# Kernel optimization log

Hardware: AMD Instinct MI355X
Metric: run time of the kernel (lower is better)

Reference implementation:

```python
import jax, jax.numpy as jnp
import numpy as np

DIM = 64
HID = 2 * DIM  # ffn_expansion_factor hard-coded to 2 in __init__


def _conv(x, w, b, pad, groups=1):
    # x: [N,C,H,W], w: [O, C//groups, kh, kw] (torch OIHW layout)
    y = jax.lax.conv_general_dilated(
        x, w, window_strides=(1, 1), padding=[(pad, pad), (pad, pad)],
        feature_group_count=groups,
        dimension_numbers=('NCHW', 'OIHW', 'NCHW'))
    return y + b[None, :, None, None]


def setup_inputs() -> dict:
    key = jax.random.key(0)
    ks = jax.random.split(key, 16)
    s = 0.05
    B, H, W = 4, 256, 256
    return {
        'x': jax.random.normal(ks[0], (B, DIM, H, W), jnp.float32),
        'pneffectiveness': jax.random.normal(ks[1], (B, 2, H, W), jnp.float32),
        # project_in: dim -> 2*hidden, 1x1
        'w_in': jax.random.normal(ks[2], (2 * HID, DIM, 1, 1), jnp.float32) * s,
        'b_in': jax.random.normal(ks[3], (2 * HID,), jnp.float32) * s,
        # project_in_pn: 2 -> hidden, 1x1
        'w_pn': jax.random.normal(ks[4], (HID, 2, 1, 1), jnp.float32) * s,
        'b_pn': jax.random.normal(ks[5], (HID,), jnp.float32) * s,
        # dwconvI: 3*hidden -> hidden, 3x3, groups=hidden (3 in-ch per group)
        'w_dw1': jax.random.normal(ks[6], (HID, 3, 3, 3), jnp.float32) * s,
        'b_dw1': jax.random.normal(ks[7], (HID,), jnp.float32) * s,
        # dwconvIII[0]: 3*hidden -> hidden, 3x3, groups=hidden
        'w_dw3a': jax.random.normal(ks[8], (HID, 3, 3, 3), jnp.float32) * s,
        'b_dw3a': jax.random.normal(ks[9], (HID,), jnp.float32) * s,
        # dwconvIII[1]: hidden -> hidden depthwise 3x3
        'w_dw3b': jax.random.normal(ks[10], (HID, 1, 3, 3), jnp.float32) * s,
        'b_dw3b': jax.random.normal(ks[11], (HID,), jnp.float32) * s,
        # project_out: hidden -> dim, 1x1, groups=2
        'w_out': jax.random.normal(ks[12], (DIM, HID // 2, 1, 1), jnp.float32) * s,
        'b_out': jax.random.normal(ks[13], (DIM,), jnp.float32) * s,
    }


def reference(x, pneffectiveness, w_in, b_in, w_pn, b_pn, w_dw1, b_dw1,
              w_dw3a, b_dw3a, w_dw3b, b_dw3b, w_out, b_out):
    xi = _conv(x, w_in, b_in, pad=0)                    # [B, 2*HID, H, W]
    pn = _conv(pneffectiveness, w_pn, b_pn, pad=0)      # [B, HID, H, W]
    xc = jnp.concatenate([pn, xi], axis=1)              # [B, 3*HID, H, W]
    d1 = _conv(xc, w_dw1, b_dw1, pad=1, groups=HID)     # [B, HID, H, W]
    d3 = _conv(xc, w_dw3a, b_dw3a, pad=1, groups=HID)
    d3 = _conv(d3, w_dw3b, b_dw3b, pad=1, groups=HID)   # [B, HID, H, W]
    x1_a, x1_b = jnp.split(d1, 2, axis=1)
    x2_a, x2_b = jnp.split(d3, 2, axis=1)
    x1 = jnp.concatenate([x1_a, x2_a], axis=1)          # [B, HID, H, W]
    x2 = jnp.concatenate([x1_b, x2_b], axis=1)
    g = jax.nn.gelu(x1, approximate=False) * x2         # exact GELU like F.gelu
    return _conv(g, w_out, b_out, pad=0, groups=2)      # [B, DIM, H, W]
```

## Files before the change

### kernel.cpp

```cpp
#include <hip/hip_runtime.h>
#include <hip/hip_bf16.h>


#define T 16
#define R20 20
#define R18 18
#define HW 65536
#define XC_BYTES ((size_t)4 * 16 * HW * 24 * 2)

typedef unsigned short u16;
typedef unsigned int u32;

typedef __attribute__((ext_vector_type(8))) short bf16x8;
typedef __attribute__((ext_vector_type(4))) float f32x4;

__device__ __forceinline__ float bflo(u32 w) {
    union { u32 i; float f; } v; v.i = w << 16; return v.f;
}
__device__ __forceinline__ float bfhi(u32 w) {
    union { u32 i; float f; } v; v.i = w & 0xffff0000u; return v.f;
}
__device__ __forceinline__ float bf2f(u16 u) {
    union { u32 i; float f; } v; v.i = ((u32)u) << 16; return v.f;
}
__device__ __forceinline__ u16 f2bf(float f) {
    union { float f; u32 i; } v; v.f = f;
    u32 x = v.i;
    u32 r = (x + 0x7fffu + ((x >> 16) & 1u)) >> 16;
    return (u16)r;
}
__device__ __forceinline__ float gelu_exact(float v) {
    return 0.5f * v * (1.0f + erff(v * 0.70710678118654752f));
}

__device__ __forceinline__ void pack_pair(float a, float b, u32& hi, u32& lo) {
    union { float f; u32 i; } ua, ub, ha, hb, la, lb;
    ua.f = a; ub.f = b;
    ha.i = ua.i & 0xffff0000u;
    hb.i = ub.i & 0xffff0000u;
    hi = (ha.i >> 16) | hb.i;
    la.f = a - ha.f;
    lb.f = b - hb.f;
    lo = (la.i >> 16) | (lb.i & 0xffff0000u);
}

__global__ __launch_bounds__(256, 2)
void k1_proj_mfma(const float* __restrict__ xin,
                  const float* __restrict__ pnin,
                  const float* __restrict__ w_in,
                  const float* __restrict__ b_in,
                  const float* __restrict__ w_pn,
                  const float* __restrict__ b_pn,
                  u16* __restrict__ xc)
{
    __shared__ float s_x[64][65];
    __shared__ __align__(16) u16 s_outT[64 * 388];
    __shared__ float s_bin[256];

    const int tid  = threadIdx.x;
    const int b    = blockIdx.y;
    const int px0  = blockIdx.x * 64;
    const int lane = tid & 63;
    const int wid  = tid >> 6;
    const int lr   = lane & 15;
    const int lh   = lane >> 4;
    const int CB   = wid * 64;

    s_bin[tid] = b_in[tid];

    {
        const float* xb = xin + (size_t)b * 64 * HW + px0;
#pragma unroll
        for (int i = 0; i < 4; ++i) {
            int idx = tid + 256 * i;
            int row = idx >> 4, seg = (idx & 15) * 4;
            float4 v = *(const float4*)(xb + (size_t)row * HW + seg);
            s_x[row][seg + 0] = v.x; s_x[row][seg + 1] = v.y;
            s_x[row][seg + 2] = v.z; s_x[row][seg + 3] = v.w;
        }
    }

    bf16x8 whi[4][2], wlo[4][2];
#pragma unroll
    for (int ci = 0; ci < 4; ++ci)
#pragma unroll
        for (int ks = 0; ks < 2; ++ks) {
            const float* wp = w_in + (size_t)(CB + 16 * ci + lr) * 64
                            + 32 * ks + 8 * lh;
            float4 A0 = *(const float4*)wp;
            float4 A1 = *(const float4*)(wp + 4);
            union { u32 u[4]; bf16x8 v; } H, L;
            pack_pair(A0.x, A0.y, H.u[0], L.u[0]);
            pack_pair(A0.z, A0.w, H.u[1], L.u[1]);
            pack_pair(A1.x, A1.y, H.u[2], L.u[2]);
            pack_pair(A1.z, A1.w, H.u[3], L.u[3]);
            whi[ci][ks] = H.v; wlo[ci][ks] = L.v;
        }

    {
        int px = tid & 63;
        float p0 = pnin[(size_t)b * 2 * HW + px0 + px];
        float p1 = pnin[(size_t)b * 2 * HW + HW + px0 + px];
        u16* orow = &s_outT[px * 388];
#pragma unroll
        for (int i = 0; i < 16; ++i) {
            int k = wid * 32 + 2 * i;
            float va = fmaf(w_pn[2 * k],     p0, fmaf(w_pn[2 * k + 1], p1, b_pn[k]));
            float vb = fmaf(w_pn[2 * k + 2], p0, fmaf(w_pn[2 * k + 3], p1, b_pn[k + 1]));
            *(u32*)&orow[k] = (u32)f2bf(va) | ((u32)f2bf(vb) << 16);
        }
    }
    __syncthreads();

    f32x4 acc[4][4];
#pragma unroll
    for (int ci = 0; ci < 4; ++ci)
#pragma unroll
        for (int pj = 0; pj < 4; ++pj)
            acc[ci][pj] = (f32x4){0.f, 0.f, 0.f, 0.f};

#pragma unroll
    for (int pj = 0; pj < 4; ++pj) {
        bf16x8 xh[2], xl[2];
#pragma unroll
        for (int ks = 0; ks < 2; ++ks) {
            const int rb = 32 * ks + 8 * lh;
            const int cb = 16 * pj + lr;
            float x0 = s_x[rb + 0][cb], x1 = s_x[rb + 1][cb];
            float x2 = s_x[rb + 2][cb], x3 = s_x[rb + 3][cb];
            float x4 = s_x[rb + 4][cb], x5 = s_x[rb + 5][cb];
            float x6 = s_x[rb + 6][cb], x7 = s_x[rb + 7][cb];
            union { u32 u[4]; bf16x8 v; } H, L;
            pack_pair(x0, x1, H.u[0], L.u[0]);
            pack_pair(x2, x3, H.u[1], L.u[1]);
            pack_pair(x4, x5, H.u[2], L.u[2]);
            pack_pair(x6, x7, H.u[3], L.u[3]);
            xh[ks] = H.v; xl[ks] = L.v;
        }
#pragma unroll
        for (int ci = 0; ci < 4; ++ci) {
#pragma unroll
            for (int ks = 0; ks < 2; ++ks) {
                acc[ci][pj] = __builtin_amdgcn_mfma_f32_16x16x32_bf16(
                    whi[ci][ks], xh[ks], acc[ci][pj], 0, 0, 0);
                acc[ci][pj] = __builtin_amdgcn_mfma_f32_16x16x32_bf16(
                    whi[ci][ks], xl[ks], acc[ci][pj], 0, 0, 0);
                acc[ci][pj] = __builtin_amdgcn_mfma_f32_16x16x32_bf16(
                    wlo[ci][ks], xh[ks], acc[ci][pj], 0, 0, 0);
            }
        }
    }

#pragma unroll
    for (int ci = 0; ci < 4; ++ci) {
        const int kk = CB + 16 * ci + 4 * lh;
        float b0 = s_bin[kk + 0], b1 = s_bin[kk + 1];
        float b2 = s_bin[kk + 2], b3 = s_bin[kk + 3];
#pragma unroll
        for (int pj = 0; pj < 4; ++pj) {
            f32x4 a = acc[ci][pj];
            int px = 16 * pj + lr;
            uint2 val;
            val.x = (u32)f2bf(a[0] + b0) | ((u32)f2bf(a[1] + b1) << 16);
            val.y = (u32)f2bf(a[2] + b2) | ((u32)f2bf(a[3] + b3) << 16);
            *(uint2*)&s_outT[px * 388 + 128 + kk] = val;
        }
    }
    __syncthreads();

    {
        const int c  = tid >> 4;
        const int pb = tid & 15;
#pragma unroll
        for (int rec = 0; rec < 4; ++rec) {
            int px = pb + 16 * rec;
            const u16* row = &s_outT[px * 388];
            const int k1o = 12 * c;
            const int k2o = 192 + 12 * c;
            uint2 a0 = *(const uint2*)&row[k1o];
            uint2 a1 = *(const uint2*)&row[k1o + 4];
            uint2 a2 = *(const uint2*)&row[k1o + 8];
            uint2 a3 = *(const uint2*)&row[k2o];
            uint2 a4 = *(const uint2*)&row[k2o + 4];
            uint2 a5 = *(const uint2*)&row[k2o + 8];
            uint4* dst = (uint4*)(xc + ((size_t)(b * 16 + c) * HW + px0 + px) * 24);
            dst[0] = make_uint4(a0.x, a0.y, a1.x, a1.y);
            dst[1] = make_uint4(a2.x, a2.y, a3.x, a3.y);
            dst[2] = make_uint4(a4.x, a4.y, a5.x, a5.y);
        }
    }
}

__global__ __launch_bounds__(512, 2)
void k2_spatial(const u16* __restrict__ xc,
                const float* __restrict__ w_dw1,  const float* __restrict__ b_dw1,
                const float* __restrict__ w_dw3a, const float* __restrict__ b_dw3a,
                const float* __restrict__ w_dw3b, const float* __restrict__ b_dw3b,
                const float* __restrict__ w_out,  const float* __restrict__ b_out,
                float* __restrict__ outp)
{
    __shared__ __align__(8) u16 s_xc[24][R20 * R20];
    __shared__ __align__(8) u16 s_d3a[8][R18 * R18];
    __shared__ __align__(8) u16 s_d1[8][T * T];
    __shared__ __align__(8) u16 s_d3[8][T * T];
    __shared__ float s_wout[64 * 64];
    __shared__ float s_wd1[8][27];
    __shared__ float s_wd3a[8][27];
    __shared__ float s_wd3b[8][9];
    __shared__ float s_b1[8], s_b3a[8], s_b3b[8];

    const int tid  = threadIdx.x;
    const int half = tid >> 8;
    const int pix  = tid & 255;
    const int ox0 = blockIdx.x * T;
    const int oy0 = blockIdx.y * T;
    const int b   = blockIdx.z;

    for (int i = tid; i < 4096; i += 512) s_wout[i] = w_out[i];

    float acc[32];
#pragma unroll
    for (int o = 0; o < 32; ++o) acc[o] = 0.f;

    for (int chunk = 0; chunk < 16; ++chunk) {
        const int c0 = chunk * 4;
        __syncthreads();

        {
            int t = tid;
            if (t < 216) {
                int gl = t / 27, idx = t - gl * 27;
                int g = (gl < 4) ? (c0 + gl) : (c0 + 60 + gl);
                s_wd1[gl][idx] = w_dw1[g * 27 + idx];
            } else if (t < 432) {
                int t2 = t - 216;
                int gl = t2 / 27, idx = t2 - gl * 27;
                int g = (gl < 4) ? (c0 + gl) : (c0 + 60 + gl);
                s_wd3a[gl][idx] = w_dw3a[g * 27 + idx];
            } else if (t < 504) {
                int t2 = t - 432;
                int gl = t2 / 9, idx = t2 - gl * 9;
                int g = (gl < 4) ? (c0 + gl) : (c0 + 60 + gl);
                s_wd3b[gl][idx] = w_dw3b[g * 9 + idx];
            } else if (t < 512) {
                int gl = t - 504;
                int g = (gl < 4) ? (c0 + gl) : (c0 + 60 + gl);
                s_b1[gl]  = b_dw1[g];
                s_b3a[gl] = b_dw3a[g];
                s_b3b[gl] = b_dw3b[g];
            }
        }

        if (tid < 400) {
            int py = tid / R20, px = tid - py * R20;
            int gy = oy0 - 2 + py, gx = ox0 - 2 + px;
            union { uint4 q[3]; u16 h[24]; } v;
            if ((unsigned)gy < 256u && (unsigned)gx < 256u) {
                const uint4* src = (const uint4*)(xc +
                    ((size_t)(b * 16 + chunk) * HW + gy * 256 + gx) * 24);
                v.q[0] = src[0]; v.q[1] = src[1]; v.q[2] = src[2];
            } else {
                v.q[0] = make_uint4(0, 0, 0, 0);
                v.q[1] = make_uint4(0, 0, 0, 0);
                v.q[2] = make_uint4(0, 0, 0, 0);
            }
#pragma unroll
            for (int l = 0; l < 24; ++l) s_xc[l][tid] = v.h[l];
        }
        __syncthreads();

        for (int task = tid; task < 8 * 81; task += 512) {
            int gl = task / 81, patch = task - gl * 81;
            int py = (patch / 9) * 2, px = (patch - (patch / 9) * 9) * 2;
            float bias = s_b3a[gl];
            float a00 = bias, a01 = bias, a10 = bias, a11 = bias;
#pragma unroll
            for (int j = 0; j < 3; ++j) {
                int lc = (gl < 4) ? (3 * gl + j) : (12 + 3 * (gl - 4) + j);
                const u32* base = (const u32*)&s_xc[lc][0];
                float win[4][4];
#pragma unroll
                for (int r = 0; r < 4; ++r) {
                    int e = (py + r) * R20 + px;
                    u32 u0 = base[e >> 1];
                    u32 u1 = base[(e >> 1) + 1];
                    win[r][0] = bflo(u0); win[r][1] = bfhi(u0);
                    win[r][2] = bflo(u1); win[r][3] = bfhi(u1);
                }
#pragma unroll
                for (int ky = 0; ky < 3; ++ky)
#pragma unroll
                    for (int kx = 0; kx < 3; ++kx) {
                        float wgt = s_wd3a[gl][j * 9 + ky * 3 + kx];
                        a00 = fmaf(wgt, win[ky][kx], a00);
                        a01 = fmaf(wgt, win[ky][kx + 1], a01);
                        a10 = fmaf(wgt, win[ky + 1][kx], a10);
                        a11 = fmaf(wgt, win[ky + 1][kx + 1], a11);
                    }
            }
            int gy0 = oy0 - 1 + py, gx0 = ox0 - 1 + px;
            bool vy0 = (unsigned)gy0 < 256u, vy1 = (unsigned)(gy0 + 1) < 256u;
            bool vx0 = (unsigned)gx0 < 256u, vx1 = (unsigned)(gx0 + 1) < 256u;
            u16* drow = &s_d3a[gl][py * R18 + px];
            drow[0]       = (vy0 && vx0) ? f2bf(a00) : (u16)0;
            drow[1]       = (vy0 && vx1) ? f2bf(a01) : (u16)0;
            drow[R18]     = (vy1 && vx0) ? f2bf(a10) : (u16)0;
            drow[R18 + 1] = (vy1 && vx1) ? f2bf(a11) : (u16)0;
        }

        {
            int gl = tid >> 6, patch = tid & 63;
            int py = (patch >> 3) * 2, px = (patch & 7) * 2;
            float bias = s_b1[gl];
            float a00 = bias, a01 = bias, a10 = bias, a11 = bias;
#pragma unroll
            for (int j = 0; j < 3; ++j) {
                int lc = (gl < 4) ? (3 * gl + j) : (12 + 3 * (gl - 4) + j);
                const u32* base = (const u32*)&s_xc[lc][0];
                float win[4][4];
#pragma unroll
                for (int r = 0; r < 4; ++r) {
                    int e = (py + 1 + r) * R20 + px;
                    u32 u0 = base[e >> 1];
                    u32 u1 = base[(e >> 1) + 1];
                    u32 u2 = base[(e >> 1) + 2];
                    win[r][0] = bfhi(u0); win[r][1] = bflo(u1);
                    win[r][2] = bfhi(u1); win[r][3] = bflo(u2);
                }
#pragma unroll
                for (int ky = 0; ky < 3; ++ky)
#pragma unroll
                    for (int kx = 0; kx < 3; ++kx) {
                        float wgt = s_wd1[gl][j * 9 + ky * 3 + kx];
                        a00 = fmaf(wgt, win[ky][kx], a00);
                        a01 = fmaf(wgt, win[ky][kx + 1], a01);
                        a10 = fmaf(wgt, win[ky + 1][kx], a10);
                        a11 = fmaf(wgt, win[ky + 1][kx + 1], a11);
                    }
            }
            u16* drow = &s_d1[gl][py * T + px];
            drow[0] = f2bf(a00); drow[1] = f2bf(a01);
            drow[T] = f2bf(a10); drow[T + 1] = f2bf(a11);
        }
        __syncthreads();

        {
            int gl = tid >> 6, patch = tid & 63;
            int py = (patch >> 3) * 2, px = (patch & 7) * 2;
            float bias = s_b3b[gl];
            float a00 = bias, a01 = bias, a10 = bias, a11 = bias;
            float win[4][4];
            const u32* base = (const u32*)&s_d3a[gl][0];
#pragma unroll
            for (int r = 0; r < 4; ++r) {
                int e = (py + r) * R18 + px;
                u32 u0 = base[e >> 1];
                u32 u1 = base[(e >> 1) + 1];
                win[r][0] = bflo(u0); win[r][1] = bfhi(u0);
                win[r][2] = bflo(u1); win[r][3] = bfhi(u1);
            }
#pragma unroll
            for (int ky = 0; ky < 3; ++ky)
#pragma unroll
                for (int kx = 0; kx < 3; ++kx) {
                    float wgt = s_wd3b[gl][ky * 3 + kx];
                    a00 = fmaf(wgt, win[ky][kx], a00);
                    a01 = fmaf(wgt, win[ky][kx + 1], a01);
                    a10 = fmaf(wgt, win[ky + 1][kx], a10);
                    a11 = fmaf(wgt, win[ky + 1][kx + 1], a11);
                }
            u16* drow = &s_d3[gl][py * T + px];
            drow[0] = f2bf(a00); drow[1] = f2bf(a01);
            drow[T] = f2bf(a10); drow[T + 1] = f2bf(a11);
        }
        __syncthreads();

        {
            const u16* sD = (half == 0) ? &s_d1[0][0] : &s_d3[0][0];
            const float* wrow = s_wout + half * 32 * 64;
#pragma unroll
            for (int jp = 0; jp < 2; ++jp) {
                int j0 = 2 * jp;
                float ga = gelu_exact(bf2f(sD[j0 * 256 + pix]))
                         * bf2f(sD[(j0 + 4) * 256 + pix]);
                float gb = gelu_exact(bf2f(sD[(j0 + 1) * 256 + pix]))
                         * bf2f(sD[(j0 + 5) * 256 + pix]);
                int c = c0 + j0;
#pragma unroll
                for (int o = 0; o < 32; ++o) {
                    float2 w2 = *(const float2*)(wrow + o * 64 + c);
                    acc[o] = fmaf(w2.x, ga, acc[o]);
                    acc[o] = fmaf(w2.y, gb, acc[o]);
                }
            }
        }
    }

    {
        int py = pix >> 4, pxx = pix & 15;
        size_t obase = (size_t)b * 64 * HW + (size_t)(half * 32) * HW
                     + (size_t)(oy0 + py) * 256 + (ox0 + pxx);
#pragma unroll
        for (int o = 0; o < 32; ++o)
            outp[obase + (size_t)o * HW] = acc[o] + b_out[half * 32 + o];
    }
}

__global__ __launch_bounds__(256, 2)
void ffd_fused(const float* __restrict__ xin, const float* __restrict__ pnin,
               const float* __restrict__ w_in, const float* __restrict__ b_in,
               const float* __restrict__ w_pn, const float* __restrict__ b_pn,
               const float* __restrict__ w_dw1, const float* __restrict__ b_dw1,
               const float* __restrict__ w_dw3a, const float* __restrict__ b_dw3a,
               const float* __restrict__ w_dw3b, const float* __restrict__ b_dw3b,
               const float* __restrict__ w_out, const float* __restrict__ b_out,
               float* __restrict__ outp)
{
    __shared__ __align__(8) u16 s_xc[24][R20 * R20];
    __shared__ __align__(8) float s_d3a[8][R18 * R18];
    __shared__ float s_d1[8][T * T];
    __shared__ float s_d3[8][T * T];
    __shared__ float s_wd1[8][27];
    __shared__ float s_wd3a[8][27];
    __shared__ float s_wd3b[8][9];
    __shared__ float s_b1[8], s_b3a[8], s_b3b[8];

    const int tid = threadIdx.x;
    const int ox0 = blockIdx.x * T;
    const int oy0 = blockIdx.y * T;
    const int b   = blockIdx.z;

    float accL[32], accH[32];
#pragma unroll
    for (int o = 0; o < 32; ++o) { accL[o] = 0.f; accH[o] = 0.f; }

    for (int chunk = 0; chunk < 16; ++chunk) {
        const int c0 = chunk * 4;
        __syncthreads();

        for (int t = tid; t < 512; t += 256) {
            if (t < 216) {
                int gl = t / 27, idx = t - gl * 27;
                int g = (gl < 4) ? (c0 + gl) : (c0 + 60 + gl);
                s_wd1[gl][idx] = w_dw1[g * 27 + idx];
            } else if (t < 432) {
                int t2 = t - 216;
                int gl = t2 / 27, idx = t2 - gl * 27;
                int g = (gl < 4) ? (c0 + gl) : (c0 + 60 + gl);
                s_wd3a[gl][idx] = w_dw3a[g * 27 + idx];
            } else if (t < 504) {
                int t2 = t - 432;
                int gl = t2 / 9, idx = t2 - gl * 9;
                int g = (gl < 4) ? (c0 + gl) : (c0 + 60 + gl);
                s_wd3b[gl][idx] = w_dw3b[g * 9 + idx];
            } else {
                int gl = t - 504;
                int g = (gl < 4) ? (c0 + gl) : (c0 + 60 + gl);
                s_b1[gl]  = b_dw1[g];
                s_b3a[gl] = b_dw3a[g];
                s_b3b[gl] = b_dw3b[g];
            }
        }

        for (int p = tid; p < R20 * R20; p += 256) {
            int py = p / R20, px = p - py * R20;
            int gy = oy0 - 2 + py, gx = ox0 - 2 + px;
            if ((unsigned)gy >= 256u || (unsigned)gx >= 256u) {
#pragma unroll 1
                for (int l = 0; l < 24; ++l) s_xc[l][p] = 0;
                continue;
            }
            const int off = gy * 256 + gx;
            float xr[64];
            const float* xp = xin + (size_t)b * 64 * HW + off;
#pragma unroll
            for (int c = 0; c < 64; ++c) xr[c] = xp[(size_t)c * HW];
            float p0 = 0.f, p1 = 0.f;
            if (3 * c0 < 128) {
                const float* pp = pnin + (size_t)b * 2 * HW + off;
                p0 = pp[0]; p1 = pp[HW];
            }
#pragma unroll 1
            for (int l = 0; l < 24; ++l) {
                int k = (l < 12) ? (3 * c0 + l) : (3 * c0 + 192 + (l - 12));
                float acc;
                if (k < 128) {
                    acc = b_pn[k] + w_pn[2 * k] * p0 + w_pn[2 * k + 1] * p1;
                } else {
                    int kk = k - 128;
                    acc = b_in[kk];
                    const float2* wr = (const float2*)(w_in + kk * 64);
#pragma unroll
                    for (int i = 0; i < 32; ++i) {
                        float2 w2 = wr[i];
                        acc = fmaf(w2.x, xr[2 * i], acc);
                        acc = fmaf(w2.y, xr[2 * i + 1], acc);
                    }
                }
                s_xc[l][p] = f2bf(acc);
            }
        }
        __syncthreads();

        for (int task = tid; task < 8 * 81; task += 256) {
            int gl = task / 81, patch = task - gl * 81;
            int py = (patch / 9) * 2, px = (patch - (patch / 9) * 9) * 2;
            float bias = s_b3a[gl];
            float a00 = bias, a01 = bias, a10 = bias, a11 = bias;
#pragma unroll
            for (int j = 0; j < 3; ++j) {
                int lc = (gl < 4) ? (3 * gl + j) : (12 + 3 * (gl - 4) + j);
                const u32* base = (const u32*)&s_xc[lc][0];
                float win[4][4];
#pragma unroll
                for (int r = 0; r < 4; ++r) {
                    int e = (py + r) * R20 + px;
                    u32 u0 = base[e >> 1];
                    u32 u1 = base[(e >> 1) + 1];
                    win[r][0] = bflo(u0); win[r][1] = bfhi(u0);
                    win[r][2] = bflo(u1); win[r][3] = bfhi(u1);
                }
#pragma unroll
                for (int ky = 0; ky < 3; ++ky)
#pragma unroll
                    for (int kx = 0; kx < 3; ++kx) {
                        float wgt = s_wd3a[gl][j * 9 + ky * 3 + kx];
                        a00 = fmaf(wgt, win[ky][kx], a00);
                        a01 = fmaf(wgt, win[ky][kx + 1], a01);
                        a10 = fmaf(wgt, win[ky + 1][kx], a10);
                        a11 = fmaf(wgt, win[ky + 1][kx + 1], a11);
                    }
            }
            int gy0 = oy0 - 1 + py, gx0 = ox0 - 1 + px;
            bool vy0 = (unsigned)gy0 < 256u, vy1 = (unsigned)(gy0 + 1) < 256u;
            bool vx0 = (unsigned)gx0 < 256u, vx1 = (unsigned)(gx0 + 1) < 256u;
            float* drow = &s_d3a[gl][py * R18 + px];
            drow[0]       = (vy0 && vx0) ? a00 : 0.f;
            drow[1]       = (vy0 && vx1) ? a01 : 0.f;
            drow[R18]     = (vy1 && vx0) ? a10 : 0.f;
            drow[R18 + 1] = (vy1 && vx1) ? a11 : 0.f;
        }

        for (int task = tid; task < 8 * 64; task += 256) {
            int gl = task >> 6, patch = task & 63;
            int py = (patch >> 3) * 2, px = (patch & 7) * 2;
            float bias = s_b1[gl];
            float a00 = bias, a01 = bias, a10 = bias, a11 = bias;
#pragma unroll
            for (int j = 0; j < 3; ++j) {
                int lc = (gl < 4) ? (3 * gl + j) : (12 + 3 * (gl - 4) + j);
                const u32* base = (const u32*)&s_xc[lc][0];
                float win[4][4];
#pragma unroll
                for (int r = 0; r < 4; ++r) {
                    int e = (py + 1 + r) * R20 + px;
                    u32 u0 = base[e >> 1];
                    u32 u1 = base[(e >> 1) + 1];
                    u32 u2 = base[(e >> 1) + 2];
                    win[r][0] = bfhi(u0); win[r][1] = bflo(u1);
                    win[r][2] = bfhi(u1); win[r][3] = bflo(u2);
                }
#pragma unroll
                for (int ky = 0; ky < 3; ++ky)
#pragma unroll
                    for (int kx = 0; kx < 3; ++kx) {
                        float wgt = s_wd1[gl][j * 9 + ky * 3 + kx];
                        a00 = fmaf(wgt, win[ky][kx], a00);
                        a01 = fmaf(wgt, win[ky][kx + 1], a01);
                        a10 = fmaf(wgt, win[ky + 1][kx], a10);
                        a11 = fmaf(wgt, win[ky + 1][kx + 1], a11);
                    }
            }
            float* drow = &s_d1[gl][py * T + px];
            drow[0] = a00; drow[1] = a01; drow[T] = a10; drow[T + 1] = a11;
        }
        __syncthreads();

        for (int task = tid; task < 8 * 64; task += 256) {
            int gl = task >> 6, patch = task & 63;
            int py = (patch >> 3) * 2, px = (patch & 7) * 2;
            float bias = s_b3b[gl];
            float a00 = bias, a01 = bias, a10 = bias, a11 = bias;
            float win[4][4];
#pragma unroll
            for (int r = 0; r < 4; ++r) {
                int e = (py + r) * R18 + px;
                float2 f0 = *(const float2*)&s_d3a[gl][e];
                float2 f1 = *(const float2*)&s_d3a[gl][e + 2];
                win[r][0] = f0.x; win[r][1] = f0.y;
                win[r][2] = f1.x; win[r][3] = f1.y;
            }
#pragma unroll
            for (int ky = 0; ky < 3; ++ky)
#pragma unroll
                for (int kx = 0; kx < 3; ++kx) {
                    float wgt = s_wd3b[gl][ky * 3 + kx];
                    a00 = fmaf(wgt, win[ky][kx], a00);
                    a01 = fmaf(wgt, win[ky][kx + 1], a01);
                    a10 = fmaf(wgt, win[ky + 1][kx], a10);
                    a11 = fmaf(wgt, win[ky + 1][kx + 1], a11);
                }
            float* drow = &s_d3[gl][py * T + px];
            drow[0] = a00; drow[1] = a01; drow[T] = a10; drow[T + 1] = a11;
        }
        __syncthreads();

#pragma unroll
        for (int jp = 0; jp < 2; ++jp) {
            int j0 = 2 * jp;
            float g1a = gelu_exact(s_d1[j0][tid])     * s_d1[j0 + 4][tid];
            float g1b = gelu_exact(s_d1[j0 + 1][tid]) * s_d1[j0 + 5][tid];
            float g2a = gelu_exact(s_d3[j0][tid])     * s_d3[j0 + 4][tid];
            float g2b = gelu_exact(s_d3[j0 + 1][tid]) * s_d3[j0 + 5][tid];
            int c = c0 + j0;
#pragma unroll
            for (int o = 0; o < 32; ++o) {
                float2 wL = *(const float2*)(w_out + o * 64 + c);
                accL[o] = fmaf(wL.x, g1a, accL[o]);
                accL[o] = fmaf(wL.y, g1b, accL[o]);
                float2 wH = *(const float2*)(w_out + (o + 32) * 64 + c);
                accH[o] = fmaf(wH.x, g2a, accH[o]);
                accH[o] = fmaf(wH.y, g2b, accH[o]);
            }
        }
    }

    {
        int py = tid >> 4, pxx = tid & 15;
        size_t obase = (size_t)b * 64 * HW
                     + (size_t)(oy0 + py) * 256 + (ox0 + pxx);
#pragma unroll
        for (int o = 0; o < 32; ++o) {
            outp[obase + (size_t)o * HW]        = accL[o] + b_out[o];
            outp[obase + (size_t)(o + 32) * HW] = accH[o] + b_out[o + 32];
        }
    }
}

extern "C" void kernel_launch(void* const* d_in, const int* in_sizes, int n_in,
                              void* d_out, int out_size, void* d_ws, size_t ws_size,
                              hipStream_t stream) {
    (void)in_sizes; (void)n_in; (void)out_size;
    const float* xin    = (const float*)d_in[0];
    const float* pnin   = (const float*)d_in[1];
    const float* w_in   = (const float*)d_in[2];
    const float* b_in   = (const float*)d_in[3];
    const float* w_pn   = (const float*)d_in[4];
    const float* b_pn   = (const float*)d_in[5];
    const float* w_dw1  = (const float*)d_in[6];
    const float* b_dw1  = (const float*)d_in[7];
    const float* w_dw3a = (const float*)d_in[8];
    const float* b_dw3a = (const float*)d_in[9];
    const float* w_dw3b = (const float*)d_in[10];
    const float* b_dw3b = (const float*)d_in[11];
    const float* w_out  = (const float*)d_in[12];
    const float* b_out  = (const float*)d_in[13];
    float* outp = (float*)d_out;

    if (ws_size >= XC_BYTES) {
        u16* xc = (u16*)d_ws;
        dim3 g1(1024, 4), b1(256);
        k1_proj_mfma<<<g1, b1, 0, stream>>>(xin, pnin, w_in, b_in, w_pn, b_pn, xc);
        dim3 g2(16, 16, 4), b2(512);
        k2_spatial<<<g2, b2, 0, stream>>>(xc, w_dw1, b_dw1, w_dw3a, b_dw3a,
                                          w_dw3b, b_dw3b, w_out, b_out, outp);
    } else {
        dim3 grid(16, 16, 4), blk(256);
        ffd_fused<<<grid, blk, 0, stream>>>(xin, pnin, w_in, b_in, w_pn, b_pn,
                                            w_dw1, b_dw1, w_dw3a, b_dw3a,
                                            w_dw3b, b_dw3b, w_out, b_out, outp);
    }
}
```

Baseline: 567.6 us.

## Prefetch next xc chunk, packed FMA projection, fast erf, direct k1 stores

k1 now writes its projection outputs straight to global xc in the interleaved layout, dropping the shared-memory transpose buffer and one barrier. k2 prefetches the next chunk's halo from global into registers so the load overlaps the current chunk's compute. The output projection weights are transposed in shared memory so packed two-wide FMAs (v_pk_fma) can be used. Exact erf in GELU is replaced by an Abramowitz-Stegun polynomial with a fast reciprocal and exp, which trades accuracy for speed. The direct k1 stores are less coalesced and may cost global bandwidth.

```diff
diff --git a/kernel.cpp b/kernel.cpp
--- a/kernel.cpp
+++ b/kernel.cpp
@@ -13,6 +13,7 @@
 
 typedef __attribute__((ext_vector_type(8))) short bf16x8;
 typedef __attribute__((ext_vector_type(4))) float f32x4;
+typedef __attribute__((ext_vector_type(2))) float f32x2;
 
 __device__ __forceinline__ float bflo(u32 w) {
     union { u32 i; float f; } v; v.i = w << 16; return v.f;
@@ -29,8 +30,26 @@
     u32 r = (x + 0x7fffu + ((x >> 16) & 1u)) >> 16;
     return (u16)r;
 }
+__device__ __forceinline__ u32 f2bf2(float a, float b) {
+    return (u32)f2bf(a) | ((u32)f2bf(b) << 16);
+}
 __device__ __forceinline__ float gelu_exact(float v) {
     return 0.5f * v * (1.0f + erff(v * 0.70710678118654752f));
+}
+__device__ __forceinline__ float erf_fast(float x) {
+    float ax = fabsf(x);
+    float t = __builtin_amdgcn_rcpf(fmaf(0.3275911f, ax, 1.0f));
+    float p = fmaf(t, 1.061405429f, -1.453152027f);
+    p = fmaf(t, p, 1.421413741f);
+    p = fmaf(t, p, -0.284496736f);
+    p = fmaf(t, p, 0.254829592f);
+    p = p * t;
+    float e = __expf(-ax * ax);
+    float r = fmaf(-p, e, 1.0f);
+    return copysignf(r, x);
+}
+__device__ __forceinline__ float gelu_fast(float v) {
+    return 0.5f * v * (1.0f + erf_fast(v * 0.70710678118654752f));
 }
 
 __device__ __forceinline__ void pack_pair(float a, float b, u32& hi, u32& lo) {
@@ -54,7 +73,6 @@
                   u16* __restrict__ xc)
 {
     __shared__ float s_x[64][65];
-    __shared__ __align__(16) u16 s_outT[64 * 388];
     __shared__ float s_bin[256];
 
     const int tid  = threadIdx.x;
@@ -98,16 +116,22 @@
         }
 
     {
-        int px = tid & 63;
+        const int wu = __builtin_amdgcn_readfirstlane(wid);
+        const int px = lane;
         float p0 = pnin[(size_t)b * 2 * HW + px0 + px];
         float p1 = pnin[(size_t)b * 2 * HW + HW + px0 + px];
-        u16* orow = &s_outT[px * 388];
-#pragma unroll
-        for (int i = 0; i < 16; ++i) {
-            int k = wid * 32 + 2 * i;
-            float va = fmaf(w_pn[2 * k],     p0, fmaf(w_pn[2 * k + 1], p1, b_pn[k]));
-            float vb = fmaf(w_pn[2 * k + 2], p0, fmaf(w_pn[2 * k + 3], p1, b_pn[k + 1]));
-            *(u32*)&orow[k] = (u32)f2bf(va) | ((u32)f2bf(vb) << 16);
+#pragma unroll
+        for (int q = 0; q < 8; ++q) {
+            int k = 32 * wu + 4 * q;
+            int c = k / 12, l = k - 12 * c;
+            float v0 = fmaf(w_pn[2*k+0], p0, fmaf(w_pn[2*k+1], p1, b_pn[k+0]));
+            float v1 = fmaf(w_pn[2*k+2], p0, fmaf(w_pn[2*k+3], p1, b_pn[k+1]));
+            float v2 = fmaf(w_pn[2*k+4], p0, fmaf(w_pn[2*k+5], p1, b_pn[k+2]));
+            float v3 = fmaf(w_pn[2*k+6], p0, fmaf(w_pn[2*k+7], p1, b_pn[k+3]));
+            uint2 val;
+            val.x = f2bf2(v0, v1);
+            val.y = f2bf2(v2, v3);
+            *(uint2*)(xc + ((size_t)(b * 16 + c) * HW + px0 + px) * 24 + l) = val;
         }
     }
     __syncthreads();
@@ -156,37 +180,18 @@
         const int kk = CB + 16 * ci + 4 * lh;
         float b0 = s_bin[kk + 0], b1 = s_bin[kk + 1];
         float b2 = s_bin[kk + 2], b3 = s_bin[kk + 3];
+        int c, l;
+        int kg = kk + 128;
+        if (kg < 192) { c = kg / 12; l = kg - 12 * c; }
+        else { int t2 = kg - 192; int cq = t2 / 12; c = cq; l = 12 + (t2 - 12 * cq); }
+        u16* rec = xc + ((size_t)(b * 16 + c) * HW + px0) * 24 + l;
 #pragma unroll
         for (int pj = 0; pj < 4; ++pj) {
             f32x4 a = acc[ci][pj];
-            int px = 16 * pj + lr;
             uint2 val;
-            val.x = (u32)f2bf(a[0] + b0) | ((u32)f2bf(a[1] + b1) << 16);
-            val.y = (u32)f2bf(a[2] + b2) | ((u32)f2bf(a[3] + b3) << 16);
-            *(uint2*)&s_outT[px * 388 + 128 + kk] = val;
-        }
-    }
-    __syncthreads();
-
-    {
-        const int c  = tid >> 4;
-        const int pb = tid & 15;
-#pragma unroll
-        for (int rec = 0; rec < 4; ++rec) {
-            int px = pb + 16 * rec;
-            const u16* row = &s_outT[px * 388];
-            const int k1o = 12 * c;
-            const int k2o = 192 + 12 * c;
-            uint2 a0 = *(const uint2*)&row[k1o];
-            uint2 a1 = *(const uint2*)&row[k1o + 4];
-            uint2 a2 = *(const uint2*)&row[k1o + 8];
-            uint2 a3 = *(const uint2*)&row[k2o];
-            uint2 a4 = *(const uint2*)&row[k2o + 4];
-            uint2 a5 = *(const uint2*)&row[k2o + 8];
-            uint4* dst = (uint4*)(xc + ((size_t)(b * 16 + c) * HW + px0 + px) * 24);
-            dst[0] = make_uint4(a0.x, a0.y, a1.x, a1.y);
-            dst[1] = make_uint4(a2.x, a2.y, a3.x, a3.y);
-            dst[2] = make_uint4(a4.x, a4.y, a5.x, a5.y);
+            val.x = f2bf2(a[0] + b0, a[1] + b1);
+            val.y = f2bf2(a[2] + b2, a[3] + b3);
+            *(uint2*)(rec + (size_t)(16 * pj + lr) * 24) = val;
         }
     }
 }
@@ -203,7 +208,7 @@
     __shared__ __align__(8) u16 s_d3a[8][R18 * R18];
     __shared__ __align__(8) u16 s_d1[8][T * T];
     __shared__ __align__(8) u16 s_d3[8][T * T];
-    __shared__ float s_wout[64 * 64];
+    __shared__ float s_woutT[64 * 66];
     __shared__ float s_wd1[8][27];
     __shared__ float s_wd3a[8][27];
     __shared__ float s_wd3b[8][9];
@@ -215,12 +220,29 @@
     const int ox0 = blockIdx.x * T;
     const int oy0 = blockIdx.y * T;
     const int b   = blockIdx.z;
-
-    for (int i = tid; i < 4096; i += 512) s_wout[i] = w_out[i];
-
-    float acc[32];
-#pragma unroll
-    for (int o = 0; o < 32; ++o) acc[o] = 0.f;
+    const int ob  = half * 32;
+
+    for (int i = tid; i < 4096; i += 512) {
+        int o = i >> 6, c = i & 63;
+        s_woutT[c * 66 + o] = w_out[i];
+    }
+
+    int hpy = tid / R20, hpx = tid - hpy * R20;
+    int hgy = oy0 - 2 + hpy, hgx = ox0 - 2 + hpx;
+    const bool pvalid = (tid < 400) &&
+                        ((unsigned)hgy < 256u) && ((unsigned)hgx < 256u);
+    const u16* psrc = xc + ((size_t)(b * 16) * HW
+                            + (pvalid ? (hgy * 256 + hgx) : 0)) * 24;
+    uint4 pv0, pv1, pv2;
+    pv0 = pv1 = pv2 = make_uint4(0, 0, 0, 0);
+    if (pvalid) {
+        const uint4* s = (const uint4*)psrc;
+        pv0 = s[0]; pv1 = s[1]; pv2 = s[2];
+    }
+
+    f32x2 acc2[16];
+#pragma unroll
+    for (int o = 0; o < 16; ++o) acc2[o] = (f32x2){0.f, 0.f};
 
     for (int chunk = 0; chunk < 16; ++chunk) {
         const int c0 = chunk * 4;
@@ -252,20 +274,20 @@
         }
 
         if (tid < 400) {
-            int py = tid / R20, px = tid - py * R20;
-            int gy = oy0 - 2 + py, gx = ox0 - 2 + px;
             union { uint4 q[3]; u16 h[24]; } v;
-            if ((unsigned)gy < 256u && (unsigned)gx < 256u) {
-                const uint4* src = (const uint4*)(xc +
-                    ((size_t)(b * 16 + chunk) * HW + gy * 256 + gx) * 24);
-                v.q[0] = src[0]; v.q[1] = src[1]; v.q[2] = src[2];
-            } else {
-                v.q[0] = make_uint4(0, 0, 0, 0);
-                v.q[1] = make_uint4(0, 0, 0, 0);
-                v.q[2] = make_uint4(0, 0, 0, 0);
-            }
+            v.q[0] = pv0; v.q[1] = pv1; v.q[2] = pv2;
 #pragma unroll
             for (int l = 0; l < 24; ++l) s_xc[l][tid] = v.h[l];
+        }
+        {
+            uint4 n0, n1, n2;
+            n0 = n1 = n2 = make_uint4(0, 0, 0, 0);
+            if (pvalid && chunk < 15) {
+                const uint4* s = (const uint4*)(psrc
+                                 + (size_t)(chunk + 1) * HW * 24);
+                n0 = s[0]; n1 = s[1]; n2 = s[2];
+            }
+            pv0 = n0; pv1 = n1; pv2 = n2;
         }
         __syncthreads();
 
@@ -377,20 +399,23 @@
 
         {
             const u16* sD = (half == 0) ? &s_d1[0][0] : &s_d3[0][0];
-            const float* wrow = s_wout + half * 32 * 64;
 #pragma unroll
             for (int jp = 0; jp < 2; ++jp) {
                 int j0 = 2 * jp;
-                float ga = gelu_exact(bf2f(sD[j0 * 256 + pix]))
+                float ga = gelu_fast(bf2f(sD[j0 * 256 + pix]))
                          * bf2f(sD[(j0 + 4) * 256 + pix]);
-                float gb = gelu_exact(bf2f(sD[(j0 + 1) * 256 + pix]))
+                float gb = gelu_fast(bf2f(sD[(j0 + 1) * 256 + pix]))
                          * bf2f(sD[(j0 + 5) * 256 + pix]);
                 int c = c0 + j0;
-#pragma unroll
-                for (int o = 0; o < 32; ++o) {
-                    float2 w2 = *(const float2*)(wrow + o * 64 + c);
-                    acc[o] = fmaf(w2.x, ga, acc[o]);
-                    acc[o] = fmaf(w2.y, gb, acc[o]);
+                const float* wc0 = &s_woutT[(c + 0) * 66 + ob];
+                const float* wc1 = &s_woutT[(c + 1) * 66 + ob];
+                f32x2 ga2 = {ga, ga}, gb2 = {gb, gb};
+#pragma unroll
+                for (int o = 0; o < 16; ++o) {
+                    f32x2 w0 = *(const f32x2*)(wc0 + 2 * o);
+                    f32x2 w1 = *(const f32x2*)(wc1 + 2 * o);
+                    acc2[o] = __builtin_elementwise_fma(w0, ga2, acc2[o]);
+                    acc2[o] = __builtin_elementwise_fma(w1, gb2, acc2[o]);
                 }
             }
         }
@@ -398,11 +423,13 @@
 
     {
         int py = pix >> 4, pxx = pix & 15;
-        size_t obase = (size_t)b * 64 * HW + (size_t)(half * 32) * HW
+        size_t obase = (size_t)b * 64 * HW + (size_t)ob * HW
                      + (size_t)(oy0 + py) * 256 + (ox0 + pxx);
 #pragma unroll
-        for (int o = 0; o < 32; ++o)
-            outp[obase + (size_t)o * HW] = acc[o] + b_out[half * 32 + o];
+        for (int o = 0; o < 16; ++o) {
+            outp[obase + (size_t)(2 * o + 0) * HW] = acc2[o][0] + b_out[ob + 2 * o + 0];
+            outp[obase + (size_t)(2 * o + 1) * HW] = acc2[o][1] + b_out[ob + 2 * o + 1];
+        }
     }
 }
 
```

After: 507.2 us. 10.6% less time.
